# Kernel tuning notes

Measured on AMD Instinct MI355X. Metric: run time of the kernel, lower is better.

## Reference

```python
import jax, jax.numpy as jnp
import numpy as np

D_MODEL = 512
NUM_HEADS = 8
D_K = D_MODEL // NUM_HEADS


def setup_inputs() -> dict:
    key = jax.random.key(0)
    ks = jax.random.split(key, 9)
    B, S = 2, 2048
    s = 1.0 / np.sqrt(D_MODEL)
    x = jax.random.normal(ks[0], (B, S, D_MODEL), dtype=jnp.float32)
    Wq = jax.random.uniform(ks[1], (D_MODEL, D_MODEL), jnp.float32, -s, s)
    bq = jax.random.uniform(ks[2], (D_MODEL,), jnp.float32, -s, s)
    Wk = jax.random.uniform(ks[3], (D_MODEL, D_MODEL), jnp.float32, -s, s)
    bk = jax.random.uniform(ks[4], (D_MODEL,), jnp.float32, -s, s)
    Wv = jax.random.uniform(ks[5], (D_MODEL, D_MODEL), jnp.float32, -s, s)
    bv = jax.random.uniform(ks[6], (D_MODEL,), jnp.float32, -s, s)
    Wo = jax.random.uniform(ks[7], (D_MODEL, D_MODEL), jnp.float32, -s, s)
    bo = jax.random.uniform(ks[8], (D_MODEL,), jnp.float32, -s, s)
    return {"x": x, "Wq": Wq, "bq": bq, "Wk": Wk, "bk": bk,
            "Wv": Wv, "bv": bv, "Wo": Wo, "bo": bo}


def reference(x, Wq, bq, Wk, bk, Wv, bv, Wo, bo):
    B, S, _ = x.shape
    # QKV projections -> [B, H, S, d_k]
    def proj(W, b):
        return (x @ W + b).reshape(B, S, NUM_HEADS, D_K).transpose(0, 2, 1, 3)
    q = proj(Wq, bq)
    k = proj(Wk, bk)
    v = proj(Wv, bv)
    # Full [B, H, S, S] scores (faithful to the original unfused attention)
    scores = jnp.einsum('bhqd,bhkd->bhqk', q, k) / jnp.sqrt(jnp.float32(D_K))
    attn = jax.nn.softmax(scores, axis=-1)  # dropout is identity in eval mode
    context = jnp.einsum('bhqk,bhkd->bhqd', attn, v)
    context = context.transpose(0, 2, 1, 3).reshape(B, S, D_MODEL)
    return context @ Wo + bo
```

## Files before the change

### kernel.cpp

```cpp
#include <hip/hip_runtime.h>
#include <hip/hip_bf16.h>

typedef __attribute__((ext_vector_type(8))) short bf16x8_t;
typedef __attribute__((ext_vector_type(4))) short short4_t;
typedef __attribute__((ext_vector_type(4))) float f32x4_t;
typedef __hip_bfloat16 bf16;

#define DM    512
#define SEQ   2048
#define NH    8
#define DKH   64
#define MTOT  4096
#define QBLK  64
#define KVBLK 128

__device__ __forceinline__ bf16x8_t frag8(const bf16* p) {
    short4_t lo = *(const short4_t*)p;
    short4_t hi = *(const short4_t*)(p + 16);
    return __builtin_shufflevector(lo, hi, 0, 1, 2, 3, 4, 5, 6, 7);
}

__device__ __forceinline__ bf16x8_t frag8_swz(const bf16* sm, int row, int stride_b, int ebase) {
    const int s  = (row & 7) << 4;
    const char* p = (const char*)sm;
    const int b0 = (row * stride_b + ebase * 2) ^ s;
    const int b1 = (row * stride_b + ebase * 2 + 32) ^ s;
    short4_t lo = *(const short4_t*)(p + b0);
    short4_t hi = *(const short4_t*)(p + b1);
    return __builtin_shufflevector(lo, hi, 0, 1, 2, 3, 4, 5, 6, 7);
}

__device__ __forceinline__ void gload_lds16(const bf16* g, bf16* s) {
    __builtin_amdgcn_global_load_lds(
        (const __attribute__((address_space(1))) unsigned int*)g,
        (__attribute__((address_space(3))) unsigned int*)s, 16, 0, 0);
}

__device__ __forceinline__ bf16x8_t pack_pa(const f32x4_t a, const f32x4_t b) {
    bf16 t[8];
    #pragma unroll
    for (int j = 0; j < 4; ++j) t[j]     = __float2bfloat16(a[j]);
    #pragma unroll
    for (int j = 0; j < 4; ++j) t[4 + j] = __float2bfloat16(b[j]);
    return *(bf16x8_t*)t;
}

__global__ __launch_bounds__(256) void cvt_x(const float* __restrict__ in,
                                             bf16* __restrict__ out, int n4) {
    const int t = blockIdx.x * blockDim.x + threadIdx.x;
    if (t < n4) {
        const float4 v = ((const float4*)in)[t];
        bf16 o[4] = { __float2bfloat16(v.x), __float2bfloat16(v.y),
                      __float2bfloat16(v.z), __float2bfloat16(v.w) };
        ((short4_t*)out)[t] = *(short4_t*)o;
    }
}

__global__ __launch_bounds__(256) void transpose_w(
    const float* __restrict__ Wq, const float* __restrict__ Wk,
    const float* __restrict__ Wv, const float* __restrict__ Wo,
    bf16* __restrict__ WT)
{
    const int z = blockIdx.z;
    const float* W = (z == 0) ? Wq : (z == 1) ? Wk : (z == 2) ? Wv : Wo;
    bf16* T = WT + (size_t)z * DM * DM;
    __shared__ bf16 t[32][33];
    const int tx = threadIdx.x, ty = threadIdx.y;
    const int x0 = blockIdx.x * 32, y0 = blockIdx.y * 32;
    #pragma unroll
    for (int i = ty; i < 32; i += 8)
        t[i][tx] = __float2bfloat16(W[(size_t)(y0 + i) * DM + x0 + tx]);
    __syncthreads();
    #pragma unroll
    for (int i = ty; i < 32; i += 8)
        T[(size_t)(x0 + i) * DM + y0 + tx] = t[tx][i];
}

__device__ __forceinline__ void gemm128_core(
    const bf16* __restrict__ A, const bf16* __restrict__ Bt,
    int rowBase, int colBase, bf16* Asm, bf16* Bsm, f32x4_t acc[4][4])
{
    const int tid = threadIdx.x;
    const int w = tid >> 6, l = tid & 63, lg = l >> 4, lr = l & 15;
    const int wm = w >> 1, wn = w & 1;
    for (int kb = 0; kb < DM; kb += 64) {
        __syncthreads();
        #pragma unroll
        for (int j = 0; j < 4; ++j) {
            const int c = tid + 256 * j;
            const int row = c >> 3, cc = (((c & 7) ^ (row & 7)) << 3);
            gload_lds16(&A [(size_t)(rowBase + row) * DM + kb + cc], Asm + c * 8);
            gload_lds16(&Bt[(size_t)(colBase + row) * DM + kb + cc], Bsm + c * 8);
        }
        __syncthreads();
        #pragma unroll
        for (int ks = 0; ks < 2; ++ks) {
            bf16x8_t af[4], bfr[4];
            #pragma unroll
            for (int m = 0; m < 4; ++m) af[m]  = frag8_swz(Asm, wm * 64 + m * 16 + lr, 128, ks * 32 + lg * 4);
            #pragma unroll
            for (int n = 0; n < 4; ++n) bfr[n] = frag8_swz(Bsm, wn * 64 + n * 16 + lr, 128, ks * 32 + lg * 4);
            #pragma unroll
            for (int m = 0; m < 4; ++m)
                #pragma unroll
                for (int n = 0; n < 4; ++n)
                    acc[m][n] = __builtin_amdgcn_mfma_f32_16x16x32_bf16(af[m], bfr[n], acc[m][n], 0, 0, 0);
        }
    }
}

__global__ __launch_bounds__(256) void qkv_proj(
    const bf16* __restrict__ X, const bf16* __restrict__ WTall,
    const float* __restrict__ bq, const float* __restrict__ bk, const float* __restrict__ bv,
    bf16* __restrict__ Qo, bf16* __restrict__ Ko, bf16* __restrict__ Vto)
{
    __shared__ bf16 Asm[8192], Bsm[8192];
    f32x4_t acc[4][4] = {};
    const int rowBase = blockIdx.y * 128, colBase = blockIdx.x * 128;
    gemm128_core(X, WTall, rowBase, colBase, Asm, Bsm, acc);

    const int tid = threadIdx.x, w = tid >> 6, l = tid & 63, lg = l >> 4, lr = l & 15;
    const int wm = w >> 1, wn = w & 1;
    #pragma unroll
    for (int n = 0; n < 4; ++n) {
        const int c = colBase + wn * 64 + n * 16 + lr;
        const int z = c >> 9, cc = c & 511, h = cc >> 6, d = cc & 63;
        const float bb = (z == 0 ? bq : z == 1 ? bk : bv)[cc];
        #pragma unroll
        for (int m = 0; m < 4; ++m)
            #pragma unroll
            for (int i = 0; i < 4; ++i) {
                const int r = rowBase + wm * 64 + m * 16 + lg * 4 + i;
                const int b = r >> 11, s = r & 2047;
                const float v = acc[m][n][i] + bb;
                if (z == 0)
                    Qo[(((size_t)(b * NH + h)) * SEQ + s) * DKH + d] = __float2bfloat16(v * 0.125f);
                else if (z == 1)
                    Ko[(((size_t)(b * NH + h)) * SEQ + s) * DKH + d] = __float2bfloat16(v);
                else
                    Vto[(((size_t)(b * NH + h)) * DKH + d) * SEQ + s] = __float2bfloat16(v);
            }
    }
}

__global__ __launch_bounds__(256) void attn(
    const bf16* __restrict__ Q, const bf16* __restrict__ K,
    const bf16* __restrict__ VT, bf16* __restrict__ Ctx)
{
    __shared__ bf16 sm[4 * 8192];

    const int bh = blockIdx.y;
    const int qb = blockIdx.x * QBLK;
    const int tid = threadIdx.x, w = tid >> 6, l = tid & 63, lg = l >> 4, lr = l & 15;
    const size_t hbase = (size_t)bh * SEQ * DKH;
    const bf16* Qh = Q + hbase;
    const bf16* Kh = K + hbase;
    const bf16* Vh = VT + hbase;

    bf16x8_t qf[2];
    {
        const bf16* qp = Qh + (size_t)(qb + w * 16 + lr) * DKH;
        qf[0] = frag8(qp + lg * 4);
        qf[1] = frag8(qp + 32 + lg * 4);
    }

    f32x4_t Oacc[4] = {};
    float mrow = -1e30f, lsum = 0.f;

    const int kr = tid >> 3, kc = (((tid & 7) ^ (kr & 7)) << 3);
    const int vr = tid >> 4, vc = (((tid & 15) ^ (vr & 7)) << 3);

    #pragma unroll
    for (int j = 0; j < 4; ++j)
        gload_lds16(&Kh[(size_t)(kr + 32 * j) * DKH + kc], sm + (tid + 256 * j) * 8);
    #pragma unroll
    for (int j = 0; j < 4; ++j)
        gload_lds16(&Vh[(size_t)(vr + 16 * j) * SEQ + vc], sm + 16384 + (tid + 256 * j) * 8);
    __syncthreads();

    int cur = 0;
    for (int t = 0; t < SEQ / KVBLK; ++t) {
        bf16* Kc = sm + cur * 8192;
        bf16* Vc = sm + 16384 + cur * 8192;

        if (t < SEQ / KVBLK - 1) {
            const int kb = (t + 1) * KVBLK;
            bf16* Kn = sm + (cur ^ 1) * 8192;
            bf16* Vn = sm + 16384 + (cur ^ 1) * 8192;
            #pragma unroll
            for (int j = 0; j < 4; ++j)
                gload_lds16(&Kh[(size_t)(kb + kr + 32 * j) * DKH + kc], Kn + (tid + 256 * j) * 8);
            #pragma unroll
            for (int j = 0; j < 4; ++j)
                gload_lds16(&Vh[(size_t)(vr + 16 * j) * SEQ + kb + vc], Vn + (tid + 256 * j) * 8);
        }

        f32x4_t sacc[8] = {};
        #pragma unroll
        for (int nf = 0; nf < 8; ++nf) {
            const int r = nf * 16 + lr;
            bf16x8_t k0 = frag8_swz(Kc, r, 128, lg * 4);
            bf16x8_t k1 = frag8_swz(Kc, r, 128, 32 + lg * 4);
            sacc[nf] = __builtin_amdgcn_mfma_f32_16x16x32_bf16(k0, qf[0], sacc[nf], 0, 0, 0);
            sacc[nf] = __builtin_amdgcn_mfma_f32_16x16x32_bf16(k1, qf[1], sacc[nf], 0, 0, 0);
        }

        float m = sacc[0][0];
        #pragma unroll
        for (int nf = 0; nf < 8; ++nf)
            #pragma unroll
            for (int i = 0; i < 4; ++i) m = fmaxf(m, sacc[nf][i]);
        m = fmaxf(m, __shfl_xor(m, 16));
        m = fmaxf(m, __shfl_xor(m, 32));
        const float mnew  = fmaxf(mrow, m);
        const float alpha = __expf(mrow - mnew);
        mrow = mnew;
        float rs = 0.f;
        #pragma unroll
        for (int nf = 0; nf < 8; ++nf)
            #pragma unroll
            for (int i = 0; i < 4; ++i) {
                const float p = __expf(sacc[nf][i] - mnew);
                sacc[nf][i] = p;
                rs += p;
            }
        rs += __shfl_xor(rs, 16);
        rs += __shfl_xor(rs, 32);
        lsum = lsum * alpha + rs;

        #pragma unroll
        for (int i = 0; i < 4; ++i) {
            const float a_i = __shfl(alpha, (l & 48) | (lg * 4 + i));
            #pragma unroll
            for (int nf = 0; nf < 4; ++nf) Oacc[nf][i] *= a_i;
        }

        #pragma unroll
        for (int ks = 0; ks < 4; ++ks) {
            const bf16x8_t pf = pack_pa(sacc[2 * ks], sacc[2 * ks + 1]);
            #pragma unroll
            for (int nf = 0; nf < 4; ++nf) {
                bf16x8_t vf = frag8_swz(Vc, nf * 16 + lr, 256, ks * 32 + lg * 4);
                Oacc[nf] = __builtin_amdgcn_mfma_f32_16x16x32_bf16(pf, vf, Oacc[nf], 0, 0, 0);
            }
        }

        __syncthreads();
        cur ^= 1;
    }

    const int b = bh >> 3, h = bh & 7;
    #pragma unroll
    for (int i = 0; i < 4; ++i) {
        const float l_i = __shfl(lsum, (l & 48) | (lg * 4 + i));
        const float inv = 1.0f / l_i;
        const int s = qb + w * 16 + lg * 4 + i;
        #pragma unroll
        for (int nf = 0; nf < 4; ++nf) {
            const int d = nf * 16 + lr;
            Ctx[(((size_t)b * SEQ + s) * NH + h) * DKH + d] = __float2bfloat16(Oacc[nf][i] * inv);
        }
    }
}

__global__ __launch_bounds__(256) void out_proj(
    const bf16* __restrict__ X, const bf16* __restrict__ Bt,
    const float* __restrict__ bias, float* __restrict__ Out)
{
    __shared__ bf16 Asm[8192], Bsm[8192];
    f32x4_t acc[4][4] = {};
    const int rowBase = blockIdx.y * 128, colBase = blockIdx.x * 128;
    gemm128_core(X, Bt, rowBase, colBase, Asm, Bsm, acc);

    const int tid = threadIdx.x, w = tid >> 6, l = tid & 63, lg = l >> 4, lr = l & 15;
    const int wm = w >> 1, wn = w & 1;
    #pragma unroll
    for (int n = 0; n < 4; ++n) {
        const int c = colBase + wn * 64 + n * 16 + lr;
        const float bb = bias[c];
        #pragma unroll
        for (int m = 0; m < 4; ++m)
            #pragma unroll
            for (int i = 0; i < 4; ++i) {
                const int r = rowBase + wm * 64 + m * 16 + lg * 4 + i;
                Out[(size_t)r * DM + c] = acc[m][n][i] + bb;
            }
    }
}

extern "C" void kernel_launch(void* const* d_in, const int* in_sizes, int n_in,
                              void* d_out, int out_size, void* d_ws, size_t ws_size,
                              hipStream_t stream) {
    const float* x  = (const float*)d_in[0];
    const float* Wq = (const float*)d_in[1];
    const float* bq = (const float*)d_in[2];
    const float* Wk = (const float*)d_in[3];
    const float* bk = (const float*)d_in[4];
    const float* Wv = (const float*)d_in[5];
    const float* bv = (const float*)d_in[6];
    const float* Wo = (const float*)d_in[7];
    const float* bo = (const float*)d_in[8];
    float* out = (float*)d_out;

    bf16* ws  = (bf16*)d_ws;
    bf16* WT  = ws;
    bf16* Xb  = ws + 1048576;
    bf16* Qw  = ws + 1048576 + 1 * 2097152;
    bf16* Kw  = ws + 1048576 + 2 * 2097152;
    bf16* VTw = ws + 1048576 + 3 * 2097152;
    bf16* Ctx = ws + 1048576 + 4 * 2097152;

    cvt_x<<<dim3(2048), 256, 0, stream>>>(x, Xb, MTOT * DM / 4);
    transpose_w<<<dim3(16, 16, 4), dim3(32, 8), 0, stream>>>(Wq, Wk, Wv, Wo, WT);
    qkv_proj<<<dim3(12, 32), 256, 0, stream>>>(Xb, WT, bq, bk, bv, Qw, Kw, VTw);
    attn<<<dim3(SEQ / QBLK, 16), 256, 0, stream>>>(Qw, Kw, VTw, Ctx);
    out_proj<<<dim3(4, 32), 256, 0, stream>>>(Ctx, WT + (size_t)3 * DM * DM, bo, out);
}
```

Measured before the change: 152.2 us.

## Shrink GEMM tiles, fold log2e into Q scale, use exp2 and transposed PV MFMA

The projection GEMMs move from 128x128 to 64x64 tiles with more blocks, which raises parallelism on the many-CU device at the cost of less reuse per block. Fragment loads switch to contiguous 16-byte reads in place of split 8-byte pairs, and the Q scale now includes log2(e) so softmax can use exp2f. The attention PV MFMA swaps its operands so each lane owns a whole row, which removes the alpha and lsum shuffles and allows vectorized context stores. It also adds s_setprio around the MFMA sections, tree-reduces the max and sum, and vectorizes the V^T store.

```diff
diff --git a/kernel.cpp b/kernel.cpp
--- a/kernel.cpp
+++ b/kernel.cpp
@@ -13,11 +13,11 @@
 #define MTOT  4096
 #define QBLK  64
 #define KVBLK 128
-
-__device__ __forceinline__ bf16x8_t frag8(const bf16* p) {
-    short4_t lo = *(const short4_t*)p;
-    short4_t hi = *(const short4_t*)(p + 16);
-    return __builtin_shufflevector(lo, hi, 0, 1, 2, 3, 4, 5, 6, 7);
+#define QSCALE 0.180336884f
+
+__device__ __forceinline__ bf16x8_t frag16_swz(const bf16* sm, int row, int stride_b, int kbyte) {
+    const int b = (row * stride_b + kbyte) ^ ((row & 7) << 4);
+    return *(const bf16x8_t*)((const char*)sm + b);
 }
 
 __device__ __forceinline__ bf16x8_t frag8_swz(const bf16* sm, int row, int stride_b, int ebase) {
@@ -45,6 +45,13 @@
     return *(bf16x8_t*)t;
 }
 
+__device__ __forceinline__ short4_t cvt4(const f32x4_t v, float scale) {
+    short4_t r;
+    #pragma unroll
+    for (int i = 0; i < 4; ++i) ((bf16*)&r)[i] = __float2bfloat16(v[i] * scale);
+    return r;
+}
+
 __global__ __launch_bounds__(256) void cvt_x(const float* __restrict__ in,
                                              bf16* __restrict__ out, int n4) {
     const int t = blockIdx.x * blockDim.x + threadIdx.x;
@@ -76,9 +83,9 @@
         T[(size_t)(x0 + i) * DM + y0 + tx] = t[tx][i];
 }
 
-__device__ __forceinline__ void gemm128_core(
+__device__ __forceinline__ void gemm64_core(
     const bf16* __restrict__ A, const bf16* __restrict__ Bt,
-    int rowBase, int colBase, bf16* Asm, bf16* Bsm, f32x4_t acc[4][4])
+    int rowBase, int colBase, bf16* Asm, bf16* Bsm, f32x4_t acc[2][2])
 {
     const int tid = threadIdx.x;
     const int w = tid >> 6, l = tid & 63, lg = l >> 4, lr = l & 15;
@@ -86,7 +93,7 @@
     for (int kb = 0; kb < DM; kb += 64) {
         __syncthreads();
         #pragma unroll
-        for (int j = 0; j < 4; ++j) {
+        for (int j = 0; j < 2; ++j) {
             const int c = tid + 256 * j;
             const int row = c >> 3, cc = (((c & 7) ^ (row & 7)) << 3);
             gload_lds16(&A [(size_t)(rowBase + row) * DM + kb + cc], Asm + c * 8);
@@ -95,15 +102,15 @@
         __syncthreads();
         #pragma unroll
         for (int ks = 0; ks < 2; ++ks) {
-            bf16x8_t af[4], bfr[4];
-            #pragma unroll
-            for (int m = 0; m < 4; ++m) af[m]  = frag8_swz(Asm, wm * 64 + m * 16 + lr, 128, ks * 32 + lg * 4);
-            #pragma unroll
-            for (int n = 0; n < 4; ++n) bfr[n] = frag8_swz(Bsm, wn * 64 + n * 16 + lr, 128, ks * 32 + lg * 4);
-            #pragma unroll
-            for (int m = 0; m < 4; ++m)
+            bf16x8_t af[2], bfr[2];
+            #pragma unroll
+            for (int m = 0; m < 2; ++m) af[m]  = frag16_swz(Asm, wm * 32 + m * 16 + lr, 128, ks * 64 + lg * 16);
+            #pragma unroll
+            for (int n = 0; n < 2; ++n) bfr[n] = frag16_swz(Bsm, wn * 32 + n * 16 + lr, 128, ks * 64 + lg * 16);
+            #pragma unroll
+            for (int m = 0; m < 2; ++m)
                 #pragma unroll
-                for (int n = 0; n < 4; ++n)
+                for (int n = 0; n < 2; ++n)
                     acc[m][n] = __builtin_amdgcn_mfma_f32_16x16x32_bf16(af[m], bfr[n], acc[m][n], 0, 0, 0);
         }
     }
@@ -114,32 +121,38 @@
     const float* __restrict__ bq, const float* __restrict__ bk, const float* __restrict__ bv,
     bf16* __restrict__ Qo, bf16* __restrict__ Ko, bf16* __restrict__ Vto)
 {
-    __shared__ bf16 Asm[8192], Bsm[8192];
-    f32x4_t acc[4][4] = {};
-    const int rowBase = blockIdx.y * 128, colBase = blockIdx.x * 128;
-    gemm128_core(X, WTall, rowBase, colBase, Asm, Bsm, acc);
+    __shared__ bf16 Asm[4096], Bsm[4096];
+    f32x4_t acc[2][2] = {};
+    const int rowBase = blockIdx.y * 64, colBase = blockIdx.x * 64;
+    gemm64_core(X, WTall, rowBase, colBase, Asm, Bsm, acc);
 
     const int tid = threadIdx.x, w = tid >> 6, l = tid & 63, lg = l >> 4, lr = l & 15;
     const int wm = w >> 1, wn = w & 1;
     #pragma unroll
-    for (int n = 0; n < 4; ++n) {
-        const int c = colBase + wn * 64 + n * 16 + lr;
+    for (int n = 0; n < 2; ++n) {
+        const int c = colBase + wn * 32 + n * 16 + lr;
         const int z = c >> 9, cc = c & 511, h = cc >> 6, d = cc & 63;
         const float bb = (z == 0 ? bq : z == 1 ? bk : bv)[cc];
         #pragma unroll
-        for (int m = 0; m < 4; ++m)
-            #pragma unroll
-            for (int i = 0; i < 4; ++i) {
-                const int r = rowBase + wm * 64 + m * 16 + lg * 4 + i;
-                const int b = r >> 11, s = r & 2047;
-                const float v = acc[m][n][i] + bb;
-                if (z == 0)
-                    Qo[(((size_t)(b * NH + h)) * SEQ + s) * DKH + d] = __float2bfloat16(v * 0.125f);
-                else if (z == 1)
-                    Ko[(((size_t)(b * NH + h)) * SEQ + s) * DKH + d] = __float2bfloat16(v);
-                else
-                    Vto[(((size_t)(b * NH + h)) * DKH + d) * SEQ + s] = __float2bfloat16(v);
+        for (int m = 0; m < 2; ++m) {
+            const int r0 = rowBase + wm * 32 + m * 16 + lg * 4;
+            const int b = r0 >> 11, s0 = r0 & 2047;
+            if (z == 2) {
+                f32x4_t v = acc[m][n];
+                #pragma unroll
+                for (int i = 0; i < 4; ++i) v[i] += bb;
+                *(short4_t*)&Vto[(((size_t)(b * NH + h)) * DKH + d) * SEQ + s0] = cvt4(v, 1.0f);
+            } else {
+                #pragma unroll
+                for (int i = 0; i < 4; ++i) {
+                    const float v = acc[m][n][i] + bb;
+                    if (z == 0)
+                        Qo[(((size_t)(b * NH + h)) * SEQ + s0 + i) * DKH + d] = __float2bfloat16(v * QSCALE);
+                    else
+                        Ko[(((size_t)(b * NH + h)) * SEQ + s0 + i) * DKH + d] = __float2bfloat16(v);
+                }
             }
+        }
     }
 }
 
@@ -160,8 +173,8 @@
     bf16x8_t qf[2];
     {
         const bf16* qp = Qh + (size_t)(qb + w * 16 + lr) * DKH;
-        qf[0] = frag8(qp + lg * 4);
-        qf[1] = frag8(qp + 32 + lg * 4);
+        qf[0] = *(const bf16x8_t*)(qp + lg * 8);
+        qf[1] = *(const bf16x8_t*)(qp + 32 + lg * 8);
     }
 
     f32x4_t Oacc[4] = {};
@@ -196,93 +209,92 @@
         }
 
         f32x4_t sacc[8] = {};
+        __builtin_amdgcn_s_setprio(1);
         #pragma unroll
         for (int nf = 0; nf < 8; ++nf) {
             const int r = nf * 16 + lr;
-            bf16x8_t k0 = frag8_swz(Kc, r, 128, lg * 4);
-            bf16x8_t k1 = frag8_swz(Kc, r, 128, 32 + lg * 4);
+            bf16x8_t k0 = frag16_swz(Kc, r, 128, lg * 16);
+            bf16x8_t k1 = frag16_swz(Kc, r, 128, 64 + lg * 16);
             sacc[nf] = __builtin_amdgcn_mfma_f32_16x16x32_bf16(k0, qf[0], sacc[nf], 0, 0, 0);
             sacc[nf] = __builtin_amdgcn_mfma_f32_16x16x32_bf16(k1, qf[1], sacc[nf], 0, 0, 0);
         }
-
-        float m = sacc[0][0];
+        __builtin_amdgcn_s_setprio(0);
+
+        float mm[8];
         #pragma unroll
         for (int nf = 0; nf < 8; ++nf)
-            #pragma unroll
-            for (int i = 0; i < 4; ++i) m = fmaxf(m, sacc[nf][i]);
+            mm[nf] = fmaxf(fmaxf(sacc[nf][0], sacc[nf][1]), fmaxf(sacc[nf][2], sacc[nf][3]));
+        #pragma unroll
+        for (int nf = 0; nf < 4; ++nf) mm[nf] = fmaxf(mm[nf], mm[nf + 4]);
+        float m = fmaxf(fmaxf(mm[0], mm[1]), fmaxf(mm[2], mm[3]));
         m = fmaxf(m, __shfl_xor(m, 16));
         m = fmaxf(m, __shfl_xor(m, 32));
         const float mnew  = fmaxf(mrow, m);
-        const float alpha = __expf(mrow - mnew);
+        const float alpha = exp2f(mrow - mnew);
         mrow = mnew;
-        float rs = 0.f;
-        #pragma unroll
-        for (int nf = 0; nf < 8; ++nf)
-            #pragma unroll
-            for (int i = 0; i < 4; ++i) {
-                const float p = __expf(sacc[nf][i] - mnew);
-                sacc[nf][i] = p;
-                rs += p;
-            }
+        float rsn[8];
+        #pragma unroll
+        for (int nf = 0; nf < 8; ++nf) {
+            #pragma unroll
+            for (int i = 0; i < 4; ++i) sacc[nf][i] = exp2f(sacc[nf][i] - mnew);
+            rsn[nf] = (sacc[nf][0] + sacc[nf][1]) + (sacc[nf][2] + sacc[nf][3]);
+        }
+        #pragma unroll
+        for (int nf = 0; nf < 4; ++nf) rsn[nf] += rsn[nf + 4];
+        float rs = (rsn[0] + rsn[1]) + (rsn[2] + rsn[3]);
         rs += __shfl_xor(rs, 16);
         rs += __shfl_xor(rs, 32);
         lsum = lsum * alpha + rs;
-
-        #pragma unroll
-        for (int i = 0; i < 4; ++i) {
-            const float a_i = __shfl(alpha, (l & 48) | (lg * 4 + i));
-            #pragma unroll
-            for (int nf = 0; nf < 4; ++nf) Oacc[nf][i] *= a_i;
-        }
-
+        #pragma unroll
+        for (int nf = 0; nf < 4; ++nf)
+            #pragma unroll
+            for (int i = 0; i < 4; ++i) Oacc[nf][i] *= alpha;
+
+        __builtin_amdgcn_s_setprio(1);
         #pragma unroll
         for (int ks = 0; ks < 4; ++ks) {
             const bf16x8_t pf = pack_pa(sacc[2 * ks], sacc[2 * ks + 1]);
             #pragma unroll
             for (int nf = 0; nf < 4; ++nf) {
                 bf16x8_t vf = frag8_swz(Vc, nf * 16 + lr, 256, ks * 32 + lg * 4);
-                Oacc[nf] = __builtin_amdgcn_mfma_f32_16x16x32_bf16(pf, vf, Oacc[nf], 0, 0, 0);
+                Oacc[nf] = __builtin_amdgcn_mfma_f32_16x16x32_bf16(vf, pf, Oacc[nf], 0, 0, 0);
             }
         }
+        __builtin_amdgcn_s_setprio(0);
 
         __syncthreads();
         cur ^= 1;
     }
 
     const int b = bh >> 3, h = bh & 7;
-    #pragma unroll
-    for (int i = 0; i < 4; ++i) {
-        const float l_i = __shfl(lsum, (l & 48) | (lg * 4 + i));
-        const float inv = 1.0f / l_i;
-        const int s = qb + w * 16 + lg * 4 + i;
-        #pragma unroll
-        for (int nf = 0; nf < 4; ++nf) {
-            const int d = nf * 16 + lr;
-            Ctx[(((size_t)b * SEQ + s) * NH + h) * DKH + d] = __float2bfloat16(Oacc[nf][i] * inv);
-        }
-    }
+    const float inv = 1.0f / lsum;
+    const int s = qb + w * 16 + lr;
+    bf16* cp = Ctx + (((size_t)b * SEQ + s) * NH + h) * DKH + lg * 4;
+    #pragma unroll
+    for (int nf = 0; nf < 4; ++nf)
+        *(short4_t*)(cp + nf * 16) = cvt4(Oacc[nf], inv);
 }
 
 __global__ __launch_bounds__(256) void out_proj(
     const bf16* __restrict__ X, const bf16* __restrict__ Bt,
     const float* __restrict__ bias, float* __restrict__ Out)
 {
-    __shared__ bf16 Asm[8192], Bsm[8192];
-    f32x4_t acc[4][4] = {};
-    const int rowBase = blockIdx.y * 128, colBase = blockIdx.x * 128;
-    gemm128_core(X, Bt, rowBase, colBase, Asm, Bsm, acc);
+    __shared__ bf16 Asm[4096], Bsm[4096];
+    f32x4_t acc[2][2] = {};
+    const int rowBase = blockIdx.y * 64, colBase = blockIdx.x * 64;
+    gemm64_core(X, Bt, rowBase, colBase, Asm, Bsm, acc);
 
     const int tid = threadIdx.x, w = tid >> 6, l = tid & 63, lg = l >> 4, lr = l & 15;
     const int wm = w >> 1, wn = w & 1;
     #pragma unroll
-    for (int n = 0; n < 4; ++n) {
-        const int c = colBase + wn * 64 + n * 16 + lr;
+    for (int n = 0; n < 2; ++n) {
+        const int c = colBase + wn * 32 + n * 16 + lr;
         const float bb = bias[c];
         #pragma unroll
-        for (int m = 0; m < 4; ++m)
+        for (int m = 0; m < 2; ++m)
             #pragma unroll
             for (int i = 0; i < 4; ++i) {
-                const int r = rowBase + wm * 64 + m * 16 + lg * 4 + i;
+                const int r = rowBase + wm * 32 + m * 16 + lg * 4 + i;
                 Out[(size_t)r * DM + c] = acc[m][n][i] + bb;
             }
     }
@@ -312,7 +324,7 @@
 
     cvt_x<<<dim3(2048), 256, 0, stream>>>(x, Xb, MTOT * DM / 4);
     transpose_w<<<dim3(16, 16, 4), dim3(32, 8), 0, stream>>>(Wq, Wk, Wv, Wo, WT);
-    qkv_proj<<<dim3(12, 32), 256, 0, stream>>>(Xb, WT, bq, bk, bv, Qw, Kw, VTw);
+    qkv_proj<<<dim3(24, 64), 256, 0, stream>>>(Xb, WT, bq, bk, bv, Qw, Kw, VTw);
     attn<<<dim3(SEQ / QBLK, 16), 256, 0, stream>>>(Qw, Kw, VTw, Ctx);
-    out_proj<<<dim3(4, 32), 256, 0, stream>>>(Ctx, WT + (size_t)3 * DM * DM, bo, out);
-}
+    out_proj<<<dim3(8, 64), 256, 0, stream>>>(Ctx, WT + (size_t)3 * DM * DM, bo, out);
+}
```

Result: faster. 141.5 us (-7.0%).
